# Kernel optimization log

Hardware: AMD Instinct MI355X
Metric: run time of the kernel (lower is better)

## Reference

```python
import jax, jax.numpy as jnp
import numpy as np

H = 2048  # hidden_size
B = 16    # batch
S = 2048  # source (values) length
T = 16    # decoder state length per layer
L = 1     # num_layers


def setup_inputs() -> dict:
    key = jax.random.key(0)
    ks = jax.random.split(key, 6)
    sc = 1.0 / np.sqrt(H)
    return {
        "query": jax.random.normal(ks[0], (L, B, T, H), dtype=jnp.float32),
        "values": jax.random.normal(ks[1], (B, S, H), dtype=jnp.float32),
        "mask": jnp.ones((B, S), dtype=jnp.bool_),  # unused by the module
        "W1_w": jax.random.normal(ks[2], (H, H), dtype=jnp.float32) * sc,
        "W1_b": jnp.zeros((H,), dtype=jnp.float32),
        "W2_w": jax.random.normal(ks[3], (H, H), dtype=jnp.float32) * sc,
        "W2_b": jnp.zeros((H,), dtype=jnp.float32),
        "V_w": jax.random.normal(ks[4], (H,), dtype=jnp.float32) * sc,
        "V_b": jnp.zeros((), dtype=jnp.float32),
    }


def reference(query, values, mask, W1_w, W1_b, W2_w, W2_b, V_w, V_b):
    # query: (L,B,T,H); non-bidirectional path keeps last time step of layer 0
    q = query[0][:, -1:, :]                        # (B,1,H)
    q_proj = q @ W1_w.T + W1_b                     # (B,1,H)
    # Faithful quirk of the source: W2 is applied to values[0] (batch elem 0)
    v_proj = values[0] @ W2_w.T + W2_b             # (S,H)
    # broadcast add -> (B,S,H), tanh, project with V -> (B,S)
    scores = jnp.tanh(q_proj + v_proj[None, :, :]) @ V_w + V_b  # (B,S)
    scores = scores[:, None, :]                    # (B,1,S)
    alphas = jax.nn.softmax(scores, axis=-1)       # (B,1,S)
    context = jnp.einsum('bqs,bsh->bqh', alphas, values)  # (B,1,H)
    return context, alphas
```

## Files before the change

### kernel.cpp

```cpp
#include <hip/hip_runtime.h>
#include <stdint.h>

#define H 2048
#define B 16
#define S 2048
#define SCH 32
#define SPC (S / SCH)

typedef __attribute__((ext_vector_type(4))) float f32x4;
typedef __attribute__((ext_vector_type(8))) __bf16 bf16x8;
typedef __attribute__((ext_vector_type(4))) short s16x4;

__device__ inline unsigned short f2bf(float f) {
    uint32_t u = __builtin_bit_cast(uint32_t, f);
    uint32_t r = (u + 0x7FFFu + ((u >> 16) & 1u)) >> 16;
    return (unsigned short)r;
}

__device__ inline void global_load_lds16(const unsigned short* g, unsigned short* l) {
    __builtin_amdgcn_global_load_lds(
        (const __attribute__((address_space(1))) void*)g,
        (__attribute__((address_space(3))) void*)l, 16, 0, 0);
}

__global__ __launch_bounds__(256) void convert2_kernel(
    const float* __restrict__ v0, const float* __restrict__ w2,
    unsigned short* __restrict__ Vb, unsigned short* __restrict__ W2b)
{
    const int n4 = (S * H) / 4;
    int i = blockIdx.x * blockDim.x + threadIdx.x;
    int stride = gridDim.x * blockDim.x;
    for (; i < 2 * n4; i += stride) {
        const float* src = (i < n4) ? v0 : w2;
        unsigned short* dst = (i < n4) ? Vb : W2b;
        int j = (i < n4) ? i : i - n4;
        f32x4 v = ((const f32x4*)src)[j];
        s16x4 o;
        #pragma unroll
        for (int k = 0; k < 4; ++k) o[k] = (short)f2bf(v[k]);
        ((s16x4*)dst)[j] = o;
    }
}

__global__ __launch_bounds__(256) void qproj_kernel(
    const float* __restrict__ query,
    const float* __restrict__ w1,
    const float* __restrict__ w1b,
    const float* __restrict__ w2b,
    float* __restrict__ qproj)
{
    int wid = threadIdx.x >> 6;
    int lane = threadIdx.x & 63;
    int h = blockIdx.x * 4 + wid;
    float acc[B];
    #pragma unroll
    for (int b = 0; b < B; ++b) acc[b] = 0.f;
    const float* wrow = w1 + (int64_t)h * H;
    for (int kc = 0; kc < H; kc += 256) {
        f32x4 w4 = *(const f32x4*)(wrow + kc + lane * 4);
        #pragma unroll
        for (int b = 0; b < B; ++b) {
            const float* q = query + ((int64_t)(b * 16 + 15)) * H + kc + lane * 4;
            f32x4 q4 = *(const f32x4*)q;
            acc[b] += w4.x * q4.x + w4.y * q4.y + w4.z * q4.z + w4.w * q4.w;
        }
    }
    #pragma unroll
    for (int b = 0; b < B; ++b) {
        float v = acc[b];
        #pragma unroll
        for (int off = 32; off > 0; off >>= 1) v += __shfl_down(v, off, 64);
        if (lane == 0) qproj[b * H + h] = v + w1b[h] + w2b[h];
    }
}

#define GM 64
#define GN 128
#define GK 64
#define NT (H / GK)

__global__ __launch_bounds__(256) void gemm_bt_kernel(
    const unsigned short* __restrict__ A,
    const unsigned short* __restrict__ Bm,
    float* __restrict__ C)
{
    __shared__ unsigned short smA[3][GM * GK];
    __shared__ unsigned short smB[3][GN * GK];

    int t = threadIdx.x;
    int lane = t & 63;
    int wid = t >> 6;
    int wr = wid >> 1, wc = wid & 1;
    int brow = blockIdx.y * GM;
    int bcol = blockIdx.x * GN;
    int l15 = lane & 15;

    f32x4 acc[2][4] = {};

    int srow = t >> 3;
    int kslot = (t & 7) ^ (srow & 7);
    const unsigned short* gA = A + (int64_t)(brow + srow) * H + kslot * 8;
    const unsigned short* gB = Bm + (int64_t)(bcol + srow) * H + kslot * 8;

    unsigned short* pA0 = smA[0]; unsigned short* pB0 = smB[0];
    unsigned short* pA1 = smA[1]; unsigned short* pB1 = smB[1];
    unsigned short* pA2 = smA[2]; unsigned short* pB2 = smB[2];

#define STAGE(pa, pb, koff) do {                                        \
        global_load_lds16(gA + (koff), (pa) + t * 8);                   \
        global_load_lds16(gA + 32 * H + (koff), (pa) + (t + 256) * 8);  \
        global_load_lds16(gB + (koff), (pb) + t * 8);                   \
        global_load_lds16(gB + 32 * H + (koff), (pb) + (t + 256) * 8);  \
        global_load_lds16(gB + 64 * H + (koff), (pb) + (t + 512) * 8);  \
        global_load_lds16(gB + 96 * H + (koff), (pb) + (t + 768) * 8);  \
    } while (0)

    int swz = (((lane >> 4) ^ (lane & 7)) << 3);

    STAGE(pA0, pB0, 0);
    STAGE(pA1, pB1, GK);
    asm volatile("s_waitcnt vmcnt(6)" ::: "memory");
    __builtin_amdgcn_s_barrier();
    __builtin_amdgcn_sched_barrier(0);

    for (int kt = 0; kt < NT; ++kt) {
        int kn = (kt + 2) * GK;
        if (kn < H) STAGE(pA2, pB2, kn);
        #pragma unroll
        for (int kk = 0; kk < 2; ++kk) {
            int sw = swz ^ (kk << 5);
            bf16x8 a[2], b[4];
            #pragma unroll
            for (int m = 0; m < 2; ++m)
                a[m] = *(const bf16x8*)&pA0[(wr * 32 + m * 16 + l15) * GK + sw];
            #pragma unroll
            for (int n = 0; n < 4; ++n)
                b[n] = *(const bf16x8*)&pB0[(wc * 64 + n * 16 + l15) * GK + sw];
            #pragma unroll
            for (int m = 0; m < 2; ++m)
                #pragma unroll
                for (int n = 0; n < 4; ++n)
                    acc[m][n] = __builtin_amdgcn_mfma_f32_16x16x32_bf16(a[m], b[n], acc[m][n], 0, 0, 0);
        }
        if (kn < H) asm volatile("s_waitcnt vmcnt(6)" ::: "memory");
        else        asm volatile("s_waitcnt vmcnt(0)" ::: "memory");
        __builtin_amdgcn_s_barrier();
        __builtin_amdgcn_sched_barrier(0);
        unsigned short* tmp;
        tmp = pA0; pA0 = pA1; pA1 = pA2; pA2 = tmp;
        tmp = pB0; pB0 = pB1; pB1 = pB2; pB2 = tmp;
    }
#undef STAGE

    #pragma unroll
    for (int m = 0; m < 2; ++m) {
        #pragma unroll
        for (int n = 0; n < 4; ++n) {
            int col = bcol + wc * 64 + n * 16 + l15;
            #pragma unroll
            for (int q = 0; q < 4; ++q) {
                int row = brow + wr * 32 + m * 16 + (lane >> 4) * 4 + q;
                C[(int64_t)row * H + col] = acc[m][n][q];
            }
        }
    }
}

#define K2LOG2E 2.8853900817779268f

__global__ __launch_bounds__(256) void scores_kernel(
    const float* __restrict__ vproj,
    const float* __restrict__ qproj,
    const float* __restrict__ vw,
    float* __restrict__ scores)
{
    int wid = threadIdx.x >> 6, lane = threadIdx.x & 63;
    int s = blockIdx.x * 4 + wid;
    float acc[B];
    #pragma unroll
    for (int b = 0; b < B; ++b) acc[b] = 0.f;
    const float* vrow = vproj + (int64_t)s * H;
    for (int hc = 0; hc < H; hc += 256) {
        f32x4 vp = *(const f32x4*)(vrow + hc + lane * 4);
        f32x4 w4 = *(const f32x4*)(vw + hc + lane * 4);
        #pragma unroll
        for (int b = 0; b < B; ++b) {
            f32x4 q4 = *(const f32x4*)(qproj + b * H + hc + lane * 4);
            #pragma unroll
            for (int j = 0; j < 4; ++j) {
                float x = q4[j] + vp[j];
                float e = __builtin_amdgcn_exp2f(x * K2LOG2E);
                float r = __builtin_amdgcn_rcpf(e + 1.0f);
                acc[b] = fmaf(w4[j], r, acc[b]);
            }
        }
    }
    #pragma unroll
    for (int b = 0; b < B; ++b) {
        float v = acc[b];
        #pragma unroll
        for (int off = 32; off > 0; off >>= 1) v += __shfl_down(v, off, 64);
        if (lane == 0) scores[b * S + s] = -2.0f * v;
    }
}

__global__ __launch_bounds__(256) void context_partial_kernel(
    const float* __restrict__ values,
    const float* __restrict__ scores,
    float* __restrict__ alphas,
    float* __restrict__ partial)
{
    __shared__ float red[8];
    __shared__ float a_lds[SPC];
    int ht = blockIdx.x;
    int sc = blockIdx.y;
    int b  = blockIdx.z;
    int t = threadIdx.x, wid = t >> 6, lane = t & 63;

    const float* srow = scores + b * S;
    float v[8];
    float m = -1e30f;
    #pragma unroll
    for (int i = 0; i < 8; ++i) { v[i] = srow[t + i * 256]; m = fmaxf(m, v[i]); }
    #pragma unroll
    for (int off = 32; off > 0; off >>= 1) m = fmaxf(m, __shfl_xor(m, off, 64));
    if (lane == 0) red[wid] = m;
    __syncthreads();
    m = fmaxf(fmaxf(red[0], red[1]), fmaxf(red[2], red[3]));
    float sum = 0.f;
    #pragma unroll
    for (int i = 0; i < 8; ++i) sum += __expf(v[i] - m);
    #pragma unroll
    for (int off = 32; off > 0; off >>= 1) sum += __shfl_xor(sum, off, 64);
    if (lane == 0) red[4 + wid] = sum;
    __syncthreads();
    float inv = 1.f / (red[4] + red[5] + red[6] + red[7]);

    if (t < SPC) {
        float a = __expf(srow[sc * SPC + t] - m) * inv;
        a_lds[t] = a;
        if (ht == 0) alphas[b * S + sc * SPC + t] = a;
    }
    __syncthreads();

    int h = ht * 1024 + t * 4;
    const float* vbase = values + (int64_t)b * S * H + (int64_t)sc * SPC * H + h;
    f32x4 acc0 = {}, acc1 = {};
    #pragma unroll 4
    for (int s = 0; s < SPC; s += 2) {
        float a0 = a_lds[s], a1 = a_lds[s + 1];
        f32x4 v0 = *(const f32x4*)(vbase + (int64_t)s * H);
        f32x4 v1 = *(const f32x4*)(vbase + (int64_t)(s + 1) * H);
        acc0 += a0 * v0;
        acc1 += a1 * v1;
    }
    *(f32x4*)(partial + ((int64_t)(sc * B + b)) * H + h) = acc0 + acc1;
}

__global__ __launch_bounds__(256) void context_reduce_kernel(
    const float* __restrict__ partial, float* __restrict__ out)
{
    int idx = blockIdx.x * 256 + threadIdx.x;
    int b = idx >> 11, h = idx & 2047;
    float s = 0.f;
    #pragma unroll
    for (int c = 0; c < SCH; ++c) s += partial[((int64_t)(c * B + b)) * H + h];
    out[idx] = s;
}

extern "C" void kernel_launch(void* const* d_in, const int* in_sizes, int n_in,
                              void* d_out, int out_size, void* d_ws, size_t ws_size,
                              hipStream_t stream) {
    const float* query  = (const float*)d_in[0];
    const float* values = (const float*)d_in[1];
    const float* w1w = (const float*)d_in[3];
    const float* w1b = (const float*)d_in[4];
    const float* w2w = (const float*)d_in[5];
    const float* w2b = (const float*)d_in[6];
    const float* vw  = (const float*)d_in[7];

    float* out = (float*)d_out;
    float* context = out;
    float* alphas  = out + B * H;

    float* ws = (float*)d_ws;
    float* qproj   = ws;
    float* scores  = ws + 32768;
    float* vproj   = ws + 65536;
    float* partial = vproj + (int64_t)S * H;
    unsigned short* Vb  = (unsigned short*)(partial + SCH * B * H);
    unsigned short* W2b = Vb + S * H;

    convert2_kernel<<<2048, 256, 0, stream>>>(values, w2w, Vb, W2b);
    qproj_kernel<<<H / 4, 256, 0, stream>>>(query, w1w, w1b, w2b, qproj);
    gemm_bt_kernel<<<dim3(H / GN, S / GM), 256, 0, stream>>>(Vb, W2b, vproj);
    scores_kernel<<<S / 4, 256, 0, stream>>>(vproj, qproj, vw, scores);
    context_partial_kernel<<<dim3(2, SCH, B), 256, 0, stream>>>(values, scores, alphas, partial);
    context_reduce_kernel<<<(B * H) / 256, 256, 0, stream>>>(partial, context);
}
```

Baseline: 133.1 us.

## Merge conversion with qproj, process two rows per scores wave, fuse context reduction

The bf16 conversion and the qproj GEMV now run as one launch, split across block ranges, so the two can overlap and one launch is saved. The scores kernel gives each wave two source rows, so each qproj and V load is reused twice. The context partial and reduce kernels become one kernel: each block covers 64 hidden columns over the full sequence and reduces across slots in LDS, which removes the partial buffer round trip and a launch. The trade-offs are fewer blocks in scores, more register pressure, and each context block recomputing the full softmax.

```diff
diff --git a/kernel.cpp b/kernel.cpp
--- a/kernel.cpp
+++ b/kernel.cpp
@@ -4,8 +4,6 @@
 #define H 2048
 #define B 16
 #define S 2048
-#define SCH 32
-#define SPC (S / SCH)
 
 typedef __attribute__((ext_vector_type(4))) float f32x4;
 typedef __attribute__((ext_vector_type(8))) __bf16 bf16x8;
@@ -23,54 +21,54 @@
         (__attribute__((address_space(3))) void*)l, 16, 0, 0);
 }
 
-__global__ __launch_bounds__(256) void convert2_kernel(
+#define CONVB 1536
+
+__global__ __launch_bounds__(256) void prep_kernel(
     const float* __restrict__ v0, const float* __restrict__ w2,
-    unsigned short* __restrict__ Vb, unsigned short* __restrict__ W2b)
-{
-    const int n4 = (S * H) / 4;
-    int i = blockIdx.x * blockDim.x + threadIdx.x;
-    int stride = gridDim.x * blockDim.x;
-    for (; i < 2 * n4; i += stride) {
-        const float* src = (i < n4) ? v0 : w2;
-        unsigned short* dst = (i < n4) ? Vb : W2b;
-        int j = (i < n4) ? i : i - n4;
-        f32x4 v = ((const f32x4*)src)[j];
-        s16x4 o;
-        #pragma unroll
-        for (int k = 0; k < 4; ++k) o[k] = (short)f2bf(v[k]);
-        ((s16x4*)dst)[j] = o;
-    }
-}
-
-__global__ __launch_bounds__(256) void qproj_kernel(
-    const float* __restrict__ query,
-    const float* __restrict__ w1,
-    const float* __restrict__ w1b,
-    const float* __restrict__ w2b,
+    unsigned short* __restrict__ Vb, unsigned short* __restrict__ W2b,
+    const float* __restrict__ query, const float* __restrict__ w1,
+    const float* __restrict__ w1b, const float* __restrict__ w2b,
     float* __restrict__ qproj)
 {
-    int wid = threadIdx.x >> 6;
-    int lane = threadIdx.x & 63;
-    int h = blockIdx.x * 4 + wid;
-    float acc[B];
-    #pragma unroll
-    for (int b = 0; b < B; ++b) acc[b] = 0.f;
-    const float* wrow = w1 + (int64_t)h * H;
-    for (int kc = 0; kc < H; kc += 256) {
-        f32x4 w4 = *(const f32x4*)(wrow + kc + lane * 4);
+    if (blockIdx.x < CONVB) {
+        const int n4 = (S * H) / 4;
+        int i = blockIdx.x * 256 + threadIdx.x;
+        int stride = CONVB * 256;
+        for (; i < 2 * n4; i += stride) {
+            const float* src = (i < n4) ? v0 : w2;
+            unsigned short* dst = (i < n4) ? Vb : W2b;
+            int j = (i < n4) ? i : i - n4;
+            f32x4 v = ((const f32x4*)src)[j];
+            s16x4 o;
+            #pragma unroll
+            for (int k = 0; k < 4; ++k) o[k] = (short)f2bf(v[k]);
+            ((s16x4*)dst)[j] = o;
+        }
+    } else {
+        int bid = blockIdx.x - CONVB;
+        int wid = threadIdx.x >> 6;
+        int lane = threadIdx.x & 63;
+        int h = bid * 4 + wid;
+        float acc[B];
+        #pragma unroll
+        for (int b = 0; b < B; ++b) acc[b] = 0.f;
+        const float* wrow = w1 + (int64_t)h * H;
+        for (int kc = 0; kc < H; kc += 256) {
+            f32x4 w4 = *(const f32x4*)(wrow + kc + lane * 4);
+            #pragma unroll
+            for (int b = 0; b < B; ++b) {
+                const float* q = query + ((int64_t)(b * 16 + 15)) * H + kc + lane * 4;
+                f32x4 q4 = *(const f32x4*)q;
+                acc[b] += w4.x * q4.x + w4.y * q4.y + w4.z * q4.z + w4.w * q4.w;
+            }
+        }
         #pragma unroll
         for (int b = 0; b < B; ++b) {
-            const float* q = query + ((int64_t)(b * 16 + 15)) * H + kc + lane * 4;
-            f32x4 q4 = *(const f32x4*)q;
-            acc[b] += w4.x * q4.x + w4.y * q4.y + w4.z * q4.z + w4.w * q4.w;
-        }
-    }
-    #pragma unroll
-    for (int b = 0; b < B; ++b) {
-        float v = acc[b];
-        #pragma unroll
-        for (int off = 32; off > 0; off >>= 1) v += __shfl_down(v, off, 64);
-        if (lane == 0) qproj[b * H + h] = v + w1b[h] + w2b[h];
+            float v = acc[b];
+            #pragma unroll
+            for (int off = 32; off > 0; off >>= 1) v += __shfl_down(v, off, 64);
+            if (lane == 0) qproj[b * H + h] = v + w1b[h] + w2b[h];
+        }
     }
 }
 
@@ -175,46 +173,57 @@
     float* __restrict__ scores)
 {
     int wid = threadIdx.x >> 6, lane = threadIdx.x & 63;
-    int s = blockIdx.x * 4 + wid;
-    float acc[B];
-    #pragma unroll
-    for (int b = 0; b < B; ++b) acc[b] = 0.f;
-    const float* vrow = vproj + (int64_t)s * H;
+    int s = blockIdx.x * 8 + wid * 2;
+    float acc0[B], acc1[B];
+    #pragma unroll
+    for (int b = 0; b < B; ++b) { acc0[b] = 0.f; acc1[b] = 0.f; }
+    const float* vr0 = vproj + (int64_t)s * H;
+    const float* vr1 = vr0 + H;
     for (int hc = 0; hc < H; hc += 256) {
-        f32x4 vp = *(const f32x4*)(vrow + hc + lane * 4);
-        f32x4 w4 = *(const f32x4*)(vw + hc + lane * 4);
+        int off = hc + lane * 4;
+        f32x4 vpa = *(const f32x4*)(vr0 + off);
+        f32x4 vpb = *(const f32x4*)(vr1 + off);
+        f32x4 w4  = *(const f32x4*)(vw + off);
         #pragma unroll
         for (int b = 0; b < B; ++b) {
-            f32x4 q4 = *(const f32x4*)(qproj + b * H + hc + lane * 4);
+            f32x4 q4 = *(const f32x4*)(qproj + b * H + off);
             #pragma unroll
             for (int j = 0; j < 4; ++j) {
-                float x = q4[j] + vp[j];
-                float e = __builtin_amdgcn_exp2f(x * K2LOG2E);
-                float r = __builtin_amdgcn_rcpf(e + 1.0f);
-                acc[b] = fmaf(w4[j], r, acc[b]);
+                float xa = q4[j] + vpa[j];
+                float ea = __builtin_amdgcn_exp2f(xa * K2LOG2E);
+                acc0[b] = fmaf(w4[j], __builtin_amdgcn_rcpf(ea + 1.0f), acc0[b]);
+                float xb = q4[j] + vpb[j];
+                float eb = __builtin_amdgcn_exp2f(xb * K2LOG2E);
+                acc1[b] = fmaf(w4[j], __builtin_amdgcn_rcpf(eb + 1.0f), acc1[b]);
             }
         }
     }
     #pragma unroll
     for (int b = 0; b < B; ++b) {
-        float v = acc[b];
-        #pragma unroll
-        for (int off = 32; off > 0; off >>= 1) v += __shfl_down(v, off, 64);
-        if (lane == 0) scores[b * S + s] = -2.0f * v;
-    }
-}
-
-__global__ __launch_bounds__(256) void context_partial_kernel(
+        float v0 = acc0[b], v1 = acc1[b];
+        #pragma unroll
+        for (int off = 32; off > 0; off >>= 1) {
+            v0 += __shfl_down(v0, off, 64);
+            v1 += __shfl_down(v1, off, 64);
+        }
+        if (lane == 0) {
+            scores[b * S + s]     = -2.0f * v0;
+            scores[b * S + s + 1] = -2.0f * v1;
+        }
+    }
+}
+
+__global__ __launch_bounds__(256) void context_kernel(
     const float* __restrict__ values,
     const float* __restrict__ scores,
     float* __restrict__ alphas,
-    float* __restrict__ partial)
+    float* __restrict__ context)
 {
     __shared__ float red[8];
-    __shared__ float a_lds[SPC];
-    int ht = blockIdx.x;
-    int sc = blockIdx.y;
-    int b  = blockIdx.z;
+    __shared__ float a_lds[S];
+    __shared__ f32x4 racc[16][16];
+    int hr = blockIdx.x;
+    int b  = blockIdx.y;
     int t = threadIdx.x, wid = t >> 6, lane = t & 63;
 
     const float* srow = scores + b * S;
@@ -227,45 +236,38 @@
     if (lane == 0) red[wid] = m;
     __syncthreads();
     m = fmaxf(fmaxf(red[0], red[1]), fmaxf(red[2], red[3]));
-    float sum = 0.f;
-    #pragma unroll
-    for (int i = 0; i < 8; ++i) sum += __expf(v[i] - m);
+    float e[8], sum = 0.f;
+    #pragma unroll
+    for (int i = 0; i < 8; ++i) { e[i] = __expf(v[i] - m); sum += e[i]; }
     #pragma unroll
     for (int off = 32; off > 0; off >>= 1) sum += __shfl_xor(sum, off, 64);
     if (lane == 0) red[4 + wid] = sum;
     __syncthreads();
     float inv = 1.f / (red[4] + red[5] + red[6] + red[7]);
-
-    if (t < SPC) {
-        float a = __expf(srow[sc * SPC + t] - m) * inv;
-        a_lds[t] = a;
-        if (ht == 0) alphas[b * S + sc * SPC + t] = a;
+    #pragma unroll
+    for (int i = 0; i < 8; ++i) {
+        float a = e[i] * inv;
+        a_lds[t + i * 256] = a;
+        if (hr == 0) alphas[b * S + t + i * 256] = a;
     }
     __syncthreads();
 
-    int h = ht * 1024 + t * 4;
-    const float* vbase = values + (int64_t)b * S * H + (int64_t)sc * SPC * H + h;
-    f32x4 acc0 = {}, acc1 = {};
-    #pragma unroll 4
-    for (int s = 0; s < SPC; s += 2) {
-        float a0 = a_lds[s], a1 = a_lds[s + 1];
-        f32x4 v0 = *(const f32x4*)(vbase + (int64_t)s * H);
-        f32x4 v1 = *(const f32x4*)(vbase + (int64_t)(s + 1) * H);
-        acc0 += a0 * v0;
-        acc1 += a1 * v1;
-    }
-    *(f32x4*)(partial + ((int64_t)(sc * B + b)) * H + h) = acc0 + acc1;
-}
-
-__global__ __launch_bounds__(256) void context_reduce_kernel(
-    const float* __restrict__ partial, float* __restrict__ out)
-{
-    int idx = blockIdx.x * 256 + threadIdx.x;
-    int b = idx >> 11, h = idx & 2047;
-    float s = 0.f;
-    #pragma unroll
-    for (int c = 0; c < SCH; ++c) s += partial[((int64_t)(c * B + b)) * H + h];
-    out[idx] = s;
+    int slot = t >> 4;
+    int hh = (t & 15) * 4;
+    const float* vbase = values + (int64_t)b * S * H + hr * 64 + hh;
+    int s0 = slot * 128;
+    f32x4 acc = {};
+    #pragma unroll 8
+    for (int i = 0; i < 128; ++i)
+        acc += a_lds[s0 + i] * *(const f32x4*)(vbase + (int64_t)(s0 + i) * H);
+    racc[slot][t & 15] = acc;
+    __syncthreads();
+    if (t < 16) {
+        f32x4 s4 = racc[0][t];
+        #pragma unroll
+        for (int k = 1; k < 16; ++k) s4 += racc[k][t];
+        *(f32x4*)(context + b * H + hr * 64 + t * 4) = s4;
+    }
 }
 
 extern "C" void kernel_launch(void* const* d_in, const int* in_sizes, int n_in,
@@ -287,14 +289,12 @@
     float* qproj   = ws;
     float* scores  = ws + 32768;
     float* vproj   = ws + 65536;
-    float* partial = vproj + (int64_t)S * H;
-    unsigned short* Vb  = (unsigned short*)(partial + SCH * B * H);
+    unsigned short* Vb  = (unsigned short*)(vproj + (int64_t)S * H);
     unsigned short* W2b = Vb + S * H;
 
-    convert2_kernel<<<2048, 256, 0, stream>>>(values, w2w, Vb, W2b);
-    qproj_kernel<<<H / 4, 256, 0, stream>>>(query, w1w, w1b, w2b, qproj);
+    prep_kernel<<<CONVB + 512, 256, 0, stream>>>(values, w2w, Vb, W2b,
+                                                 query, w1w, w1b, w2b, qproj);
     gemm_bt_kernel<<<dim3(H / GN, S / GM), 256, 0, stream>>>(Vb, W2b, vproj);
-    scores_kernel<<<S / 4, 256, 0, stream>>>(vproj, qproj, vw, scores);
-    context_partial_kernel<<<dim3(2, SCH, B), 256, 0, stream>>>(values, scores, alphas, partial);
-    context_reduce_kernel<<<(B * H) / 256, 256, 0, stream>>>(partial, context);
-}
+    scores_kernel<<<S / 8, 256, 0, stream>>>(vproj, qproj, vw, scores);
+    context_kernel<<<dim3(32, B), 256, 0, stream>>>(values, scores, alphas, context);
+}
```

New measurement: 166.0 us. 24.7% more time.
